# Performance work log

Measured on AMD Instinct MI355X. Metric: run time of the kernel, lower is better.

Reference implementation:

```python
import jax, jax.numpy as jnp
import numpy as np

N_HEADS = 16
HEAD_DIM = 128  # dim // n_heads = 2048 // 16

def setup_inputs() -> dict:
    key = jax.random.key(0)
    ks = jax.random.split(key, 7)
    B, S, D = 2, 2048, 2048
    scale = 0.02
    return {
        "q": jax.random.normal(ks[0], (B, S, D), dtype=jnp.float32),
        "k": jax.random.normal(ks[1], (B, S, D), dtype=jnp.float32),
        "v": jax.random.normal(ks[2], (B, S, D), dtype=jnp.float32),
        "wq": jax.random.normal(ks[3], (D, D), dtype=jnp.float32) * scale,
        "wk": jax.random.normal(ks[4], (D, D), dtype=jnp.float32) * scale,
        "wv": jax.random.normal(ks[5], (D, D), dtype=jnp.float32) * scale,
        "wo": jax.random.normal(ks[6], (D, D), dtype=jnp.float32) * scale,
    }

def reference(q, k, v, wq, wk, wv, wo):
    B, S, _ = q.shape
    # Linear (no bias): torch Linear computes x @ W.T; weights here stored as [out, in]
    xq = (q @ wq.T).reshape(B, S, N_HEADS, HEAD_DIM).transpose(0, 2, 1, 3)  # [B,H,S,d]
    xk = (k @ wk.T).reshape(B, S, N_HEADS, HEAD_DIM).transpose(0, 2, 1, 3)
    xv = (v @ wv.T).reshape(B, S, N_HEADS, HEAD_DIM).transpose(0, 2, 1, 3)
    scores = jnp.einsum("bhqd,bhkd->bhqk", xq, xk) / jnp.sqrt(jnp.float32(HEAD_DIM))
    # causal mask: -inf above the diagonal
    causal = jnp.tril(jnp.ones((S, S), dtype=bool))
    scores = jnp.where(causal[None, None], scores, -jnp.inf)
    attn = jax.nn.softmax(scores.astype(jnp.float32), axis=-1)  # dropout is identity at eval
    out = jnp.einsum("bhqk,bhkd->bhqd", attn, xv)
    out = out.transpose(0, 2, 1, 3).reshape(B, S, N_HEADS * HEAD_DIM)
    return out @ wo.T
```

## Files before the change

### kernel.cpp

```cpp
#include <hip/hip_runtime.h>
#include <hip/hip_bf16.h>

#define B_ 2
#define S_ 2048
#define D_ 2048
#define H_ 16
#define HD_ 128

typedef __attribute__((ext_vector_type(4))) float f32x4;
typedef __attribute__((ext_vector_type(8))) short bf16x8;

static __device__ __forceinline__ unsigned short f2bf(float f) {
    unsigned int u = __float_as_uint(f);
    u += 0x7fffu + ((u >> 16) & 1u);
    return (unsigned short)(u >> 16);
}
static __device__ __forceinline__ float bf2f(unsigned short h) {
    return __uint_as_float(((unsigned int)h) << 16);
}

#define MFMA_K32(a, b, c) __builtin_amdgcn_mfma_f32_16x16x32_bf16(a, b, c, 0, 0, 0)

static __device__ __forceinline__ void gll16(const void* g, void* l) {
    __builtin_amdgcn_global_load_lds((const __attribute__((address_space(1))) void*)g,
                                     (__attribute__((address_space(3))) void*)l,
                                     16, 0, 0);
}

__global__ void cvt_in(const float4* __restrict__ src, ushort4* __restrict__ dst) {
    int i = blockIdx.x * 256 + threadIdx.x;
    float4 v = src[i];
    ushort4 o;
    o.x = f2bf(v.x); o.y = f2bf(v.y); o.z = f2bf(v.z); o.w = f2bf(v.w);
    dst[i] = o;
}

__global__ void cvt_w4(const float4* __restrict__ s0, ushort4* __restrict__ d0,
                       const float4* __restrict__ s1, ushort4* __restrict__ d1,
                       const float4* __restrict__ s2, ushort4* __restrict__ d2,
                       const float4* __restrict__ s3, ushort4* __restrict__ d3) {
    const float4* s; ushort4* d;
    switch (blockIdx.y) {
        case 0: s = s0; d = d0; break;
        case 1: s = s1; d = d1; break;
        case 2: s = s2; d = d2; break;
        default: s = s3; d = d3; break;
    }
    int i = blockIdx.x * 256 + threadIdx.x;
    float4 v = s[i];
    ushort4 o;
    o.x = f2bf(v.x); o.y = f2bf(v.y); o.z = f2bf(v.z); o.w = f2bf(v.w);
    d[i] = o;
}

template<int OUT_MODE>
__global__ __launch_bounds__(256) void gemm_xwt(
        const unsigned short* __restrict__ A,
        const unsigned short* __restrict__ W,
        void* __restrict__ C) {
    constexpr int K = D_;
    __shared__ unsigned short As[2][128 * 32];
    __shared__ unsigned short Ws[2][128 * 32];
    const int tid = threadIdx.x, lane = tid & 63, wid = tid >> 6;
    const int wy = wid >> 1, wx = wid & 1;
    const int g = lane >> 4, lr = lane & 15;
    const int swz = (blockIdx.x & 7) * 64 + (blockIdx.x >> 3);
    const int bm = (swz & 31) * 128;
    const int bn = (swz >> 5) * 128;

    const int r0 = (wid * 128 + lane) >> 2, c0 = (lane & 3) * 8;
    const int r1 = r0 + 16;

    f32x4 acc[4][4] = {};

    auto stage = [&](int k0, int nb) {
        gll16(A + (size_t)(bm + r0) * K + k0 + c0, (char*)&As[nb][0] + wid * 2048);
        gll16(A + (size_t)(bm + r1) * K + k0 + c0, (char*)&As[nb][0] + wid * 2048 + 1024);
        gll16(W + (size_t)(bn + r0) * K + k0 + c0, (char*)&Ws[nb][0] + wid * 2048);
        gll16(W + (size_t)(bn + r1) * K + k0 + c0, (char*)&Ws[nb][0] + wid * 2048 + 1024);
    };

    stage(0, 0);
    int cur = 0;

    for (int k0 = 0; k0 < K; k0 += 32) {
        __syncthreads();
        if (k0 + 32 < K) stage(k0 + 32, cur ^ 1);
        bf16x8 af[4], wf[4];
        #pragma unroll
        for (int i = 0; i < 4; ++i)
            af[i] = *(const bf16x8*)((const char*)&As[cur][0] + (wy * 64 + i * 16 + lr) * 64 + g * 16);
        #pragma unroll
        for (int i = 0; i < 4; ++i)
            wf[i] = *(const bf16x8*)((const char*)&Ws[cur][0] + (wx * 64 + i * 16 + lr) * 64 + g * 16);
        #pragma unroll
        for (int mi = 0; mi < 4; ++mi)
            #pragma unroll
            for (int ni = 0; ni < 4; ++ni)
                acc[mi][ni] = MFMA_K32(af[mi], wf[ni], acc[mi][ni]);
        cur ^= 1;
    }

    #pragma unroll
    for (int mi = 0; mi < 4; ++mi) {
        #pragma unroll
        for (int ni = 0; ni < 4; ++ni) {
            const int n = bn + wx * 64 + ni * 16 + lr;
            const int m0 = bm + wy * 64 + mi * 16 + g * 4;
            if constexpr (OUT_MODE == 0) {
                #pragma unroll
                for (int rg = 0; rg < 4; ++rg) {
                    int m = m0 + rg;
                    int bb = m >> 11, s = m & (S_ - 1);
                    int hh = n >> 7, dd = n & (HD_ - 1);
                    ((unsigned short*)C)[(((size_t)(bb * H_ + hh) * S_) + s) * HD_ + dd] =
                        f2bf(acc[mi][ni][rg]);
                }
            } else if constexpr (OUT_MODE == 1) {
                #pragma unroll
                for (int rg = 0; rg < 4; ++rg) {
                    int m = m0 + rg;
                    int bb = m >> 11, s = m & (S_ - 1);
                    int hh = n >> 7, dd = n & (HD_ - 1);
                    int vr = s & 63;
                    int pr = (vr & 3) | (((vr >> 3) & 3) << 2) | (((vr >> 2) & 1) << 4) | (vr & 32);
                    size_t eo = ((size_t)(bb * H_ + hh) << 18) + ((size_t)(s >> 6) << 13)
                              + pr * 128 + (((((unsigned)dd) << 1) ^ ((pr & 7) << 4)) >> 1);
                    ((unsigned short*)C)[eo] = f2bf(acc[mi][ni][rg]);
                }
            } else if constexpr (OUT_MODE == 2) {
                int bb = m0 >> 11, s0 = m0 & (S_ - 1);
                int hh = n >> 7, dd = n & (HD_ - 1);
                int ch = ((s0 & 63) >> 3) ^ (dd & 7);
                size_t eo = ((size_t)(bb * H_ + hh) << 18) + ((size_t)(s0 >> 6) << 13)
                          + dd * 64 + (ch << 3) + (s0 & 7);
                ushort4 pk;
                pk.x = f2bf(acc[mi][ni][0]); pk.y = f2bf(acc[mi][ni][1]);
                pk.z = f2bf(acc[mi][ni][2]); pk.w = f2bf(acc[mi][ni][3]);
                *(ushort4*)&((unsigned short*)C)[eo] = pk;
            } else {
                #pragma unroll
                for (int rg = 0; rg < 4; ++rg)
                    ((float*)C)[(size_t)(m0 + rg) * D_ + n] = acc[mi][ni][rg];
            }
        }
    }
}

__global__ __launch_bounds__(128, 4) void attn_fwd(
        const unsigned short* __restrict__ Qg,
        const unsigned short* __restrict__ Kt,
        const unsigned short* __restrict__ Vt,
        unsigned short* __restrict__ Og) {
    __shared__ char Ks[16384];
    __shared__ char Vs[16384];
    const int tid = threadIdx.x, lane = tid & 63, w = tid >> 6;
    const int g = lane >> 4, lr = lane & 15;
    const int i = blockIdx.x;
    const int qi = 31 - (i >> 5);
    const int bh = i & 31;
    const int b = bh >> 4, h = bh & (H_ - 1);
    const size_t base = (size_t)bh * S_ * HD_;
    const float SCL = 0.08838834764831845f * 1.4426950408889634f;

    auto stage = [&](int t) {
        const size_t tb = base + (size_t)t * 8192 + w * 4096 + (size_t)lane * 8;
        char* kd = Ks + w * 8192;
        char* vd = Vs + w * 8192;
        #pragma unroll
        for (int c = 0; c < 8; ++c) {
            gll16(Kt + tb + c * 512, kd + c * 1024);
            gll16(Vt + tb + c * 512, vd + c * 1024);
        }
    };

    const int q0 = qi * 64;
    const int qrA = q0 + w * 16 + lr;
    const int qrB = qrA + 32;

    bf16x8 qfA[4], qfB[4];
    #pragma unroll
    for (int st = 0; st < 4; ++st) {
        bf16x8 ta = *(const bf16x8*)(Qg + base + (size_t)qrA * HD_ + st * 32 + g * 8);
        bf16x8 tb2 = *(const bf16x8*)(Qg + base + (size_t)qrB * HD_ + st * 32 + g * 8);
        #pragma unroll
        for (int jj = 0; jj < 8; ++jj) {
            ta[jj] = (short)f2bf(bf2f((unsigned short)ta[jj]) * SCL);
            tb2[jj] = (short)f2bf(bf2f((unsigned short)tb2[jj]) * SCL);
        }
        qfA[st] = ta; qfB[st] = tb2;
    }

    float mA = -1e30f, lA = 0.0f, mB = -1e30f, lB = 0.0f;
    f32x4 accA[8] = {}, accB[8] = {};
    const int nt = qi + 1;

    for (int t = 0; t < nt; ++t) {
        __syncthreads();
        stage(t);
        __syncthreads();

        f32x4 sA[4] = {}, sB[4] = {};
        __builtin_amdgcn_s_setprio(1);
        #pragma unroll
        for (int f = 0; f < 4; ++f) {
            const int row = f * 16 + lr;
            const int sw = (row & 7) << 4;
            #pragma unroll
            for (int st = 0; st < 4; ++st) {
                bf16x8 kf = *(const bf16x8*)(Ks + row * 256 + ((st * 64 + g * 16) ^ sw));
                sA[f] = MFMA_K32(kf, qfA[st], sA[f]);
                sB[f] = MFMA_K32(kf, qfB[st], sB[f]);
            }
        }
        __builtin_amdgcn_s_setprio(0);

        if (t == nt - 1) {
            #pragma unroll
            for (int f = 0; f < 4; ++f)
                #pragma unroll
                for (int rg = 0; rg < 4; ++rg) {
                    const int kv = q0 + 32 * (f >> 1) + 8 * g + 4 * (f & 1) + rg;
                    if (kv > qrA) sA[f][rg] = -1e30f;
                    if (kv > qrB) sB[f][rg] = -1e30f;
                }
        }

        bf16x8 pAlo, pAhi, pBlo, pBhi;
        auto softmax_step = [&](f32x4* sf, float& m_r, float& l_r, f32x4* accO,
                                bf16x8& plo, bf16x8& phi) {
            float pm = -1e30f;
            #pragma unroll
            for (int f = 0; f < 4; ++f)
                #pragma unroll
                for (int rg = 0; rg < 4; ++rg) pm = fmaxf(pm, sf[f][rg]);
            pm = fmaxf(pm, __shfl_xor(pm, 16));
            pm = fmaxf(pm, __shfl_xor(pm, 32));
            if (!__all(pm <= m_r + 8.0f)) {
                const float mnew = fmaxf(m_r, pm);
                const float corr = exp2f(m_r - mnew);
                m_r = mnew;
                float cj[4];
                #pragma unroll
                for (int jj = 0; jj < 4; ++jj) cj[jj] = __shfl(corr, g * 4 + jj);
                #pragma unroll
                for (int db = 0; db < 8; ++db) {
                    accO[db][0] *= cj[0]; accO[db][1] *= cj[1];
                    accO[db][2] *= cj[2]; accO[db][3] *= cj[3];
                }
                l_r *= corr;
            }
            float ls = 0.0f;
            #pragma unroll
            for (int f = 0; f < 2; ++f)
                #pragma unroll
                for (int rg = 0; rg < 4; ++rg) {
                    float pv = exp2f(sf[f][rg] - m_r);
                    ls += pv;
                    plo[f * 4 + rg] = (short)f2bf(pv);
                }
            #pragma unroll
            for (int f = 0; f < 2; ++f)
                #pragma unroll
                for (int rg = 0; rg < 4; ++rg) {
                    float pv = exp2f(sf[2 + f][rg] - m_r);
                    ls += pv;
                    phi[f * 4 + rg] = (short)f2bf(pv);
                }
            ls += __shfl_xor(ls, 16);
            ls += __shfl_xor(ls, 32);
            l_r += ls;
        };
        softmax_step(sA, mA, lA, accA, pAlo, pAhi);
        softmax_step(sB, mB, lB, accB, pBlo, pBhi);

        __builtin_amdgcn_s_setprio(1);
        #pragma unroll
        for (int db = 0; db < 8; ++db) {
            const int d = db * 16 + lr;
            bf16x8 vlo = *(const bf16x8*)(Vs + d * 128 + ((g ^ (d & 7)) << 4));
            bf16x8 vhi = *(const bf16x8*)(Vs + d * 128 + (((4 + g) ^ (d & 7)) << 4));
            accA[db] = MFMA_K32(pAlo, vlo, accA[db]);
            accA[db] = MFMA_K32(pAhi, vhi, accA[db]);
            accB[db] = MFMA_K32(pBlo, vlo, accB[db]);
            accB[db] = MFMA_K32(pBhi, vhi, accB[db]);
        }
        __builtin_amdgcn_s_setprio(0);
    }

    {
        float lj[4];
        #pragma unroll
        for (int jj = 0; jj < 4; ++jj) lj[jj] = __shfl(lA, g * 4 + jj);
        #pragma unroll
        for (int jj = 0; jj < 4; ++jj) {
            const int qq = q0 + w * 16 + g * 4 + jj;
            const float inv = 1.0f / lj[jj];
            unsigned short* dst = Og + ((size_t)(b * S_ + qq)) * D_ + h * HD_;
            #pragma unroll
            for (int db = 0; db < 8; ++db)
                dst[db * 16 + lr] = f2bf(accA[db][jj] * inv);
        }
        #pragma unroll
        for (int jj = 0; jj < 4; ++jj) lj[jj] = __shfl(lB, g * 4 + jj);
        #pragma unroll
        for (int jj = 0; jj < 4; ++jj) {
            const int qq = q0 + 32 + w * 16 + g * 4 + jj;
            const float inv = 1.0f / lj[jj];
            unsigned short* dst = Og + ((size_t)(b * S_ + qq)) * D_ + h * HD_;
            #pragma unroll
            for (int db = 0; db < 8; ++db)
                dst[db * 16 + lr] = f2bf(accB[db][jj] * inv);
        }
    }
}

extern "C" void kernel_launch(void* const* d_in, const int* in_sizes, int n_in,
                              void* d_out, int out_size, void* d_ws, size_t ws_size,
                              hipStream_t stream) {
    const float* q  = (const float*)d_in[0];
    const float* k  = (const float*)d_in[1];
    const float* v  = (const float*)d_in[2];
    const float* wq = (const float*)d_in[3];
    const float* wk = (const float*)d_in[4];
    const float* wv = (const float*)d_in[5];
    const float* wo = (const float*)d_in[6];

    unsigned short* ws   = (unsigned short*)d_ws;
    unsigned short* wqb  = ws;
    unsigned short* wkb  = wqb + (size_t)D_ * D_;
    unsigned short* wvb  = wkb + (size_t)D_ * D_;
    unsigned short* wob  = wvb + (size_t)D_ * D_;
    unsigned short* xq   = wob + (size_t)D_ * D_;
    unsigned short* xk   = xq + (size_t)B_ * S_ * D_;
    unsigned short* xv   = xk + (size_t)B_ * S_ * D_;
    unsigned short* slot = xv + (size_t)B_ * S_ * D_;

    cvt_w4<<<dim3(4096, 4), 256, 0, stream>>>(
        (const float4*)wq, (ushort4*)wqb, (const float4*)wk, (ushort4*)wkb,
        (const float4*)wv, (ushort4*)wvb, (const float4*)wo, (ushort4*)wob);

    cvt_in<<<8192, 256, 0, stream>>>((const float4*)q, (ushort4*)slot);
    gemm_xwt<0><<<512, 256, 0, stream>>>(slot, wqb, xq);
    cvt_in<<<8192, 256, 0, stream>>>((const float4*)k, (ushort4*)slot);
    gemm_xwt<1><<<512, 256, 0, stream>>>(slot, wkb, xk);
    cvt_in<<<8192, 256, 0, stream>>>((const float4*)v, (ushort4*)slot);
    gemm_xwt<2><<<512, 256, 0, stream>>>(slot, wvb, xv);

    attn_fwd<<<1024, 128, 0, stream>>>(xq, xk, xv, slot);

    gemm_xwt<3><<<512, 256, 0, stream>>>(slot, wob, d_out);
}
```

Measured before the change: 358.5 us.

## Double-buffer LDS in GEMM and attention, halve KV tile to 32 rows

The projection GEMM now prefetches two K-steps ahead into double-buffered LDS, using vmcnt waits and raw barriers in place of __syncthreads before each tile. The attention kernel splits each 64-row KV tile into two 32-row tiles with double-buffered K/V LDS, so loads overlap compute and per-block LDS drops. It also skips the A-half MFMAs on the final fully-masked tile, and the V layout swizzle is changed to match. The cost is twice the loop iterations, more barriers, and relying on hand-counted vmcnt values.

```diff
diff --git a/kernel.cpp b/kernel.cpp
--- a/kernel.cpp
+++ b/kernel.cpp
@@ -20,6 +20,7 @@
 }
 
 #define MFMA_K32(a, b, c) __builtin_amdgcn_mfma_f32_16x16x32_bf16(a, b, c, 0, 0, 0)
+#define FENCE() asm volatile("" ::: "memory")
 
 static __device__ __forceinline__ void gll16(const void* g, void* l) {
     __builtin_amdgcn_global_load_lds((const __attribute__((address_space(1))) void*)g,
@@ -81,11 +82,14 @@
     };
 
     stage(0, 0);
+    stage(32, 1);
     int cur = 0;
 
     for (int k0 = 0; k0 < K; k0 += 32) {
-        __syncthreads();
-        if (k0 + 32 < K) stage(k0 + 32, cur ^ 1);
+        if (k0 + 32 < K) asm volatile("s_waitcnt vmcnt(4)" ::: "memory");
+        else             asm volatile("s_waitcnt vmcnt(0)" ::: "memory");
+        __builtin_amdgcn_s_barrier();
+        FENCE();
         bf16x8 af[4], wf[4];
         #pragma unroll
         for (int i = 0; i < 4; ++i)
@@ -98,6 +102,10 @@
             #pragma unroll
             for (int ni = 0; ni < 4; ++ni)
                 acc[mi][ni] = MFMA_K32(af[mi], wf[ni], acc[mi][ni]);
+        FENCE();
+        __builtin_amdgcn_s_barrier();
+        FENCE();
+        if (k0 + 64 < K) stage(k0 + 64, cur);
         cur ^= 1;
     }
 
@@ -131,9 +139,9 @@
             } else if constexpr (OUT_MODE == 2) {
                 int bb = m0 >> 11, s0 = m0 & (S_ - 1);
                 int hh = n >> 7, dd = n & (HD_ - 1);
-                int ch = ((s0 & 63) >> 3) ^ (dd & 7);
-                size_t eo = ((size_t)(bb * H_ + hh) << 18) + ((size_t)(s0 >> 6) << 13)
-                          + dd * 64 + (ch << 3) + (s0 & 7);
+                int ch = ((s0 & 31) >> 3) ^ (dd & 3);
+                size_t eo = ((size_t)(bb * H_ + hh) << 18) + ((size_t)(s0 >> 5) << 12)
+                          + dd * 32 + (ch << 3) + (s0 & 7);
                 ushort4 pk;
                 pk.x = f2bf(acc[mi][ni][0]); pk.y = f2bf(acc[mi][ni][1]);
                 pk.z = f2bf(acc[mi][ni][2]); pk.w = f2bf(acc[mi][ni][3]);
@@ -152,8 +160,8 @@
         const unsigned short* __restrict__ Kt,
         const unsigned short* __restrict__ Vt,
         unsigned short* __restrict__ Og) {
-    __shared__ char Ks[16384];
-    __shared__ char Vs[16384];
+    __shared__ char Ks[2][8192];
+    __shared__ char Vs[2][8192];
     const int tid = threadIdx.x, lane = tid & 63, w = tid >> 6;
     const int g = lane >> 4, lr = lane & 15;
     const int i = blockIdx.x;
@@ -163,14 +171,19 @@
     const size_t base = (size_t)bh * S_ * HD_;
     const float SCL = 0.08838834764831845f * 1.4426950408889634f;
 
-    auto stage = [&](int t) {
-        const size_t tb = base + (size_t)t * 8192 + w * 4096 + (size_t)lane * 8;
-        char* kd = Ks + w * 8192;
-        char* vd = Vs + w * 8192;
-        #pragma unroll
-        for (int c = 0; c < 8; ++c) {
-            gll16(Kt + tb + c * 512, kd + c * 1024);
-            gll16(Vt + tb + c * 512, vd + c * 1024);
+    auto stage = [&](int t, int nb) {
+        const char* ksrc = (const char*)Kt + ((size_t)bh << 19)
+                         + ((size_t)(t >> 1) << 14) + (t & 1) * 8192 + w * 4096
+                         + (size_t)lane * 16;
+        const char* vsrc = (const char*)Vt + ((size_t)bh << 19)
+                         + ((size_t)t << 13) + w * 4096
+                         + (size_t)lane * 16;
+        char* kd = &Ks[nb][0] + w * 4096;
+        char* vd = &Vs[nb][0] + w * 4096;
+        #pragma unroll
+        for (int c = 0; c < 4; ++c) {
+            gll16(ksrc + c * 1024, kd + c * 1024);
+            gll16(vsrc + c * 1024, vd + c * 1024);
         }
     };
 
@@ -193,45 +206,57 @@
 
     float mA = -1e30f, lA = 0.0f, mB = -1e30f, lB = 0.0f;
     f32x4 accA[8] = {}, accB[8] = {};
-    const int nt = qi + 1;
+    const int nt = 2 * qi + 2;
+
+    stage(0, 0);
+    stage(1, 1);
+    int cur = 0;
 
     for (int t = 0; t < nt; ++t) {
-        __syncthreads();
-        stage(t);
-        __syncthreads();
-
-        f32x4 sA[4] = {}, sB[4] = {};
+        if (t < nt - 1) asm volatile("s_waitcnt vmcnt(8)" ::: "memory");
+        else            asm volatile("s_waitcnt vmcnt(0)" ::: "memory");
+        __builtin_amdgcn_s_barrier();
+        FENCE();
+        const char* Kb = &Ks[cur][0];
+        const char* Vb = &Vs[cur][0];
+        const bool actA = (t < nt - 1);
+
+        f32x4 sA[2] = {}, sB[2] = {};
         __builtin_amdgcn_s_setprio(1);
         #pragma unroll
-        for (int f = 0; f < 4; ++f) {
+        for (int f = 0; f < 2; ++f) {
             const int row = f * 16 + lr;
             const int sw = (row & 7) << 4;
             #pragma unroll
             for (int st = 0; st < 4; ++st) {
-                bf16x8 kf = *(const bf16x8*)(Ks + row * 256 + ((st * 64 + g * 16) ^ sw));
-                sA[f] = MFMA_K32(kf, qfA[st], sA[f]);
+                bf16x8 kf = *(const bf16x8*)(Kb + row * 256 + ((st * 64 + g * 16) ^ sw));
+                if (actA) sA[f] = MFMA_K32(kf, qfA[st], sA[f]);
                 sB[f] = MFMA_K32(kf, qfB[st], sB[f]);
             }
         }
         __builtin_amdgcn_s_setprio(0);
 
+        if (t == nt - 2) {
+            #pragma unroll
+            for (int f = 0; f < 2; ++f)
+                #pragma unroll
+                for (int rg = 0; rg < 4; ++rg)
+                    if (q0 + 8 * g + 4 * f + rg > qrA) sA[f][rg] = -1e30f;
+        }
         if (t == nt - 1) {
             #pragma unroll
-            for (int f = 0; f < 4; ++f)
-                #pragma unroll
-                for (int rg = 0; rg < 4; ++rg) {
-                    const int kv = q0 + 32 * (f >> 1) + 8 * g + 4 * (f & 1) + rg;
-                    if (kv > qrA) sA[f][rg] = -1e30f;
-                    if (kv > qrB) sB[f][rg] = -1e30f;
-                }
-        }
-
-        bf16x8 pAlo, pAhi, pBlo, pBhi;
+            for (int f = 0; f < 2; ++f)
+                #pragma unroll
+                for (int rg = 0; rg < 4; ++rg)
+                    if (q0 + 32 + 8 * g + 4 * f + rg > qrB) sB[f][rg] = -1e30f;
+        }
+
+        bf16x8 pA, pB;
         auto softmax_step = [&](f32x4* sf, float& m_r, float& l_r, f32x4* accO,
-                                bf16x8& plo, bf16x8& phi) {
+                                bf16x8& pl) {
             float pm = -1e30f;
             #pragma unroll
-            for (int f = 0; f < 4; ++f)
+            for (int f = 0; f < 2; ++f)
                 #pragma unroll
                 for (int rg = 0; rg < 4; ++rg) pm = fmaxf(pm, sf[f][rg]);
             pm = fmaxf(pm, __shfl_xor(pm, 16));
@@ -257,35 +282,30 @@
                 for (int rg = 0; rg < 4; ++rg) {
                     float pv = exp2f(sf[f][rg] - m_r);
                     ls += pv;
-                    plo[f * 4 + rg] = (short)f2bf(pv);
-                }
-            #pragma unroll
-            for (int f = 0; f < 2; ++f)
-                #pragma unroll
-                for (int rg = 0; rg < 4; ++rg) {
-                    float pv = exp2f(sf[2 + f][rg] - m_r);
-                    ls += pv;
-                    phi[f * 4 + rg] = (short)f2bf(pv);
+                    pl[f * 4 + rg] = (short)f2bf(pv);
                 }
             ls += __shfl_xor(ls, 16);
             ls += __shfl_xor(ls, 32);
             l_r += ls;
         };
-        softmax_step(sA, mA, lA, accA, pAlo, pAhi);
-        softmax_step(sB, mB, lB, accB, pBlo, pBhi);
+        if (actA) softmax_step(sA, mA, lA, accA, pA);
+        softmax_step(sB, mB, lB, accB, pB);
 
         __builtin_amdgcn_s_setprio(1);
         #pragma unroll
         for (int db = 0; db < 8; ++db) {
             const int d = db * 16 + lr;
-            bf16x8 vlo = *(const bf16x8*)(Vs + d * 128 + ((g ^ (d & 7)) << 4));
-            bf16x8 vhi = *(const bf16x8*)(Vs + d * 128 + (((4 + g) ^ (d & 7)) << 4));
-            accA[db] = MFMA_K32(pAlo, vlo, accA[db]);
-            accA[db] = MFMA_K32(pAhi, vhi, accA[db]);
-            accB[db] = MFMA_K32(pBlo, vlo, accB[db]);
-            accB[db] = MFMA_K32(pBhi, vhi, accB[db]);
+            bf16x8 vb = *(const bf16x8*)(Vb + d * 64 + ((g ^ (d & 3)) << 4));
+            if (actA) accA[db] = MFMA_K32(pA, vb, accA[db]);
+            accB[db] = MFMA_K32(pB, vb, accB[db]);
         }
         __builtin_amdgcn_s_setprio(0);
+
+        FENCE();
+        __builtin_amdgcn_s_barrier();
+        FENCE();
+        if (t + 2 < nt) stage(t + 2, cur);
+        cur ^= 1;
     }
 
     {
```

Measured after the change: 390.7 us. +9.0%, slower.
